# Performance work log

Hardware: AMD Instinct MI355X
Metric: run time of the kernel (lower is better)

## Reference

```python
import jax, jax.numpy as jnp
import numpy as np

C = 512
NUM_HEADS = 8
GROUPS = 32
EPS_GN = 1e-5
EPS_ATTN = 1e-6


def setup_inputs() -> dict:
    key = jax.random.key(0)
    ks = jax.random.split(key, 7)
    B, H, W = 8, 64, 64
    x = jax.random.normal(ks[0], (B, C, H, W), dtype=jnp.float32)
    # GroupNorm affine (torch default: weight=1, bias=0)
    norm_gamma = jnp.ones((C,), dtype=jnp.float32)
    norm_beta = jnp.zeros((C,), dtype=jnp.float32)
    # 1x1 conv weights stored as (out, in); torch Conv2d kaiming-ish scale
    qkv_w = jax.random.normal(ks[1], (3 * C, C), dtype=jnp.float32) * (1.0 / np.sqrt(C))
    qkv_b = jax.random.normal(ks[2], (3 * C,), dtype=jnp.float32) * 0.01
    proj_w = jax.random.normal(ks[3], (C, C), dtype=jnp.float32) * (1.0 / np.sqrt(C))
    proj_b = jax.random.normal(ks[4], (C,), dtype=jnp.float32) * 0.01
    return {"x": x, "norm_gamma": norm_gamma, "norm_beta": norm_beta,
            "qkv_w": qkv_w, "qkv_b": qkv_b, "proj_w": proj_w, "proj_b": proj_b}


def _group_norm(x, gamma, beta):
    B, Cc, H, W = x.shape
    xg = x.reshape(B, GROUPS, Cc // GROUPS, H, W)
    mean = xg.mean(axis=(2, 3, 4), keepdims=True)
    var = xg.var(axis=(2, 3, 4), keepdims=True)
    xn = (xg - mean) * jax.lax.rsqrt(var + EPS_GN)
    xn = xn.reshape(B, Cc, H, W)
    return xn * gamma[None, :, None, None] + beta[None, :, None, None]


def reference(x, norm_gamma, norm_beta, qkv_w, qkv_b, proj_w, proj_b):
    B, Cc, H, W = x.shape
    h, d = NUM_HEADS, Cc // NUM_HEADS
    N = H * W
    x_norm = _group_norm(x, norm_gamma, norm_beta)
    # 1x1 conv == channel GEMM
    qkv = jnp.einsum('bchw,oc->bohw', x_norm, qkv_w) + qkv_b[None, :, None, None]
    q, k, v = jnp.split(qkv, 3, axis=1)
    # (B, C, H, W) -> (B, h, N, d)
    def to_heads(t):
        return t.reshape(B, h, d, N).transpose(0, 1, 3, 2)
    q, k, v = to_heads(q), to_heads(k), to_heads(v)
    # phi(x) = elu(x) + 1
    q = jax.nn.elu(q) + 1.0
    k = jax.nn.elu(k) + 1.0
    kv = jnp.einsum('bhnd,bhne->bhde', k, v)          # (B,h,d,d)
    out = jnp.einsum('bhnd,bhde->bhne', q, kv)        # (B,h,N,d)
    denom = jnp.einsum('bhnd,bhd->bhn', q, k.sum(axis=2))
    out = out / (denom[..., None] + EPS_ATTN)
    # (B,h,N,d) -> (B,C,H,W)
    attn = out.transpose(0, 1, 3, 2).reshape(B, Cc, H, W)
    proj = jnp.einsum('bchw,oc->bohw', attn, proj_w) + proj_b[None, :, None, None]
    # dropout is identity at inference
    return x + proj
```

## Files before the change

kernel.cpp:

```cpp
#include <hip/hip_runtime.h>
#include <math.h>

#define BATCH   8
#define CCH     512
#define NHEADS  8
#define HD      64
#define NGROUPS 32
#define CPG     16
#define NSP     4096
#define O1      1536

typedef __attribute__((ext_vector_type(8))) short          short8;
typedef __attribute__((ext_vector_type(8))) unsigned short ushort8;
typedef __attribute__((ext_vector_type(4))) unsigned short ushort4v;
typedef __attribute__((ext_vector_type(4))) float          float4v;

#define GLOAD_LDS16(g, s) __builtin_amdgcn_global_load_lds(                   \
    (const __attribute__((address_space(1))) void*)(g),                       \
    (__attribute__((address_space(3))) void*)(s), 16, 0, 0)

__device__ __forceinline__ float phi_act(float v) {
    return v > 0.f ? v + 1.f : __expf(v);
}
__device__ __forceinline__ unsigned short f2bf(float f) {
    union { float f; unsigned int u; } c; c.f = f;
    unsigned int u = c.u;
    u += 0x7fffu + ((u >> 16) & 1u);
    return (unsigned short)(u >> 16);
}
__device__ __forceinline__ float bf2f(unsigned short s) {
    union { unsigned int u; float f; } c; c.u = ((unsigned int)s) << 16;
    return c.f;
}


__global__ __launch_bounds__(256) void gn_stats(const float* __restrict__ x,
                                                const float* __restrict__ gamma,
                                                const float* __restrict__ beta,
                                                float* __restrict__ ss) {
    const int bg = blockIdx.x;
    const int t  = threadIdx.x;
    const float* base = x + (size_t)bg * (CPG * NSP);
    float s = 0.f, s2 = 0.f;
    #pragma unroll 4
    for (int i = 0; i < 64; ++i) {
        float4 v = *(const float4*)(base + (i * 256 + t) * 4);
        s  += v.x + v.y + v.z + v.w;
        s2 += v.x * v.x + v.y * v.y + v.z * v.z + v.w * v.w;
    }
    __shared__ float r1[256], r2[256];
    r1[t] = s; r2[t] = s2;
    __syncthreads();
    for (int off = 128; off > 0; off >>= 1) {
        if (t < off) { r1[t] += r1[t + off]; r2[t] += r2[t + off]; }
        __syncthreads();
    }
    if (t < CPG) {
        const float inv = 1.f / 65536.f;
        float mean = r1[0] * inv;
        float var  = r2[0] * inv - mean * mean;
        float rstd = rsqrtf(var + 1e-5f);
        int b = bg / NGROUPS, g = bg % NGROUPS;
        int c = g * CPG + t;
        float sc = gamma[c] * rstd;
        float sh = beta[c] - mean * sc;
        ss[(b * CCH + c) * 2]     = sc;
        ss[(b * CCH + c) * 2 + 1] = sh;
    }
}

__global__ __launch_bounds__(256) void conv_w(const float* __restrict__ qw,
                                              const float* __restrict__ pw,
                                              unsigned short* __restrict__ qwb,
                                              unsigned short* __restrict__ pwb,
                                              float* __restrict__ ksum,
                                              float* __restrict__ den) {
    int i = (blockIdx.x * 256 + threadIdx.x) * 4;
    if (i < O1 * CCH) {
        float4 v = *(const float4*)(qw + i);
        unsigned short o[4] = {f2bf(v.x), f2bf(v.y), f2bf(v.z), f2bf(v.w)};
        *(uint2*)(qwb + i) = *(uint2*)o;
    } else {
        int j = i - O1 * CCH;
        float4 v = *(const float4*)(pw + j);
        unsigned short o[4] = {f2bf(v.x), f2bf(v.y), f2bf(v.z), f2bf(v.w)};
        *(uint2*)(pwb + j) = *(uint2*)o;
    }
    float4 z = {0.f, 0.f, 0.f, 0.f};
    if (blockIdx.x == 0) {
        #pragma unroll
        for (int l = 0; l < 4; ++l)
            *(float4*)(ksum + (l * 256 + threadIdx.x) * 4) = z;
    }
    if (blockIdx.x < 32)
        *(float4*)(den + (blockIdx.x * 256 + threadIdx.x) * 4) = z;
}

__global__ __launch_bounds__(256) void xnT_kernel(const float* __restrict__ x,
                                                  const float* __restrict__ ss,
                                                  unsigned short* __restrict__ xnT) {
    const int n0 = blockIdx.x * 64, c0 = blockIdx.y * 64, b = blockIdx.z;
    const int t = threadIdx.x;
    __shared__ float tile[64][65];
    const float* xb  = x + ((size_t)b * CCH + c0) * NSP + n0;
    const float* ssb = ss + b * CCH * 2;

    const int lr = t / 16, lc = (t % 16) * 4;
    #pragma unroll
    for (int j = 0; j < 4; ++j) {
        int cr = j * 16 + lr;
        float4 v = *(const float4*)(xb + (size_t)cr * NSP + lc);
        float sc = ssb[(c0 + cr) * 2], sh = ssb[(c0 + cr) * 2 + 1];
        tile[cr][lc + 0] = v.x * sc + sh;
        tile[cr][lc + 1] = v.y * sc + sh;
        tile[cr][lc + 2] = v.z * sc + sh;
        tile[cr][lc + 3] = v.w * sc + sh;
    }
    __syncthreads();
    #pragma unroll
    for (int j = 0; j < 2; ++j) {
        int wd = j * 256 + t;
        int n  = wd >> 3;
        int cb = (wd & 7) * 8;
        ushort8 o;
        #pragma unroll
        for (int i = 0; i < 8; ++i) o[i] = f2bf(tile[cb + i][n]);
        *(ushort8*)(xnT + ((size_t)b * NSP + n0 + n) * CCH + c0 + cb) = o;
    }
}

__global__ __launch_bounds__(256) void gemm_q(const unsigned short* __restrict__ A,
                                              const unsigned short* __restrict__ Bt,
                                              const float* __restrict__ bias,
                                              const float* __restrict__ ksum,
                                              unsigned short* __restrict__ qT,
                                              float* __restrict__ den) {
    const int n0 = blockIdx.x * 128;
    const int o0 = blockIdx.y * 128;
    const int b  = blockIdx.z;
    const int t  = threadIdx.x;
    const int wv = t >> 6, ln = t & 63;
    const int quad = ln >> 4, lm = ln & 15;
    const int wo = (wv >> 1) * 64, wn = (wv & 1) * 64;

    __shared__ __align__(16) unsigned short As[128 * 64];
    __shared__ __align__(16) unsigned short Bs[128 * 64];
    __shared__ float kss[128];

    if (t < 32)
        *(float4*)(kss + t * 4) = *(const float4*)(ksum + b * CCH + o0 + t * 4);

    float4v acc[4][4];
    #pragma unroll
    for (int i = 0; i < 4; ++i)
        #pragma unroll
        for (int j = 0; j < 4; ++j) acc[i][j] = {0.f, 0.f, 0.f, 0.f};

    const unsigned short* aBase = A + (size_t)o0 * CCH;
    const unsigned short* bBase = Bt + ((size_t)b * NSP + n0) * CCH;

    const int srow8 = ln >> 3;
    const int scs   = ((ln & 7) ^ srow8) * 8;
    const int lmp   = (lm & 7);

    for (int k0 = 0; k0 < CCH; k0 += 64) {
        __syncthreads();
        #pragma unroll
        for (int i = 0; i < 4; ++i) {
            int slab = wv + i * 4;
            GLOAD_LDS16(aBase + (size_t)(slab * 8 + srow8) * CCH + k0 + scs,
                        As + slab * 512);
            GLOAD_LDS16(bBase + (size_t)(slab * 8 + srow8) * CCH + k0 + scs,
                        Bs + slab * 512);
        }
        __syncthreads();
        #pragma unroll
        for (int kk = 0; kk < 2; ++kk) {
            const int sc8 = ((kk * 4 + quad) ^ lmp) * 8;
            short8 fw[4], fx[4];
            #pragma unroll
            for (int i = 0; i < 4; ++i)
                fw[i] = *(const short8*)(As + (wo + i * 16 + lm) * 64 + sc8);
            #pragma unroll
            for (int j = 0; j < 4; ++j)
                fx[j] = *(const short8*)(Bs + (wn + j * 16 + lm) * 64 + sc8);
            #pragma unroll
            for (int i = 0; i < 4; ++i)
                #pragma unroll
                for (int j = 0; j < 4; ++j)
                    acc[i][j] = __builtin_amdgcn_mfma_f32_16x16x32_bf16(
                        fw[i], fx[j], acc[i][j], 0, 0, 0);
        }
    }

    float denp[4] = {0.f, 0.f, 0.f, 0.f};
    #pragma unroll
    for (int i = 0; i < 4; ++i) {
        int ob = o0 + wo + i * 16 + quad * 4;
        float4 b4 = *(const float4*)(bias + ob);
        float bs[4] = {b4.x, b4.y, b4.z, b4.w};
        float4 k4 = *(const float4*)(kss + wo + i * 16 + quad * 4);
        float kf[4] = {k4.x, k4.y, k4.z, k4.w};
        #pragma unroll
        for (int j = 0; j < 4; ++j) {
            int n = n0 + wn + j * 16 + lm;
            ushort4v pk;
            #pragma unroll
            for (int r = 0; r < 4; ++r) {
                float qv = phi_act(acc[i][j][r] + bs[r]);
                pk[r] = f2bf(qv);
                denp[j] += qv * kf[r];
            }
            *(ushort4v*)(qT + ((size_t)b * NSP + n) * CCH + ob) = pk;
        }
    }
    #pragma unroll
    for (int j = 0; j < 4; ++j) {
        float s = denp[j];
        s += __shfl_xor(s, 16);
        s += __shfl_xor(s, 32);
        if (quad == 0)
            atomicAdd(den + (size_t)b * NSP + n0 + wn + j * 16 + lm, s);
    }
}

__global__ __launch_bounds__(256) void gemm_kv(const unsigned short* __restrict__ A,
                                               const unsigned short* __restrict__ Bt,
                                               const float* __restrict__ bias,
                                               float* __restrict__ ksum,
                                               float* __restrict__ kvp) {
    const int n0 = blockIdx.x * 128;
    const int h  = blockIdx.y;
    const int b  = blockIdx.z;
    const int t  = threadIdx.x;
    const int wv = t >> 6, ln = t & 63;
    const int quad = ln >> 4, lm = ln & 15;
    const int wo = (wv >> 1) * 64, wn = (wv & 1) * 64;

    __shared__ __align__(16) unsigned short sh[2 * 128 * 64];

    float4v acc[4][4];
    #pragma unroll
    for (int i = 0; i < 4; ++i)
        #pragma unroll
        for (int j = 0; j < 4; ++j) acc[i][j] = {0.f, 0.f, 0.f, 0.f};

    const unsigned short* aK = A + (size_t)(512 + h * 64) * CCH;
    const unsigned short* aV = A + (size_t)(1024 + h * 64) * CCH;
    const unsigned short* bBase = Bt + ((size_t)b * NSP + n0) * CCH;

    const int srow8 = ln >> 3;
    const int scs   = ((ln & 7) ^ srow8) * 8;
    const int lmp   = (lm & 7);

    for (int k0 = 0; k0 < CCH; k0 += 64) {
        __syncthreads();
        #pragma unroll
        for (int i = 0; i < 4; ++i) {
            int slab = wv + i * 4;
            const unsigned short* ab = (slab < 8)
                ? aK + (size_t)(slab * 8 + srow8) * CCH
                : aV + (size_t)((slab - 8) * 8 + srow8) * CCH;
            GLOAD_LDS16(ab + k0 + scs, sh + slab * 512);
            GLOAD_LDS16(bBase + (size_t)(slab * 8 + srow8) * CCH + k0 + scs,
                        sh + 8192 + slab * 512);
        }
        __syncthreads();
        #pragma unroll
        for (int kk = 0; kk < 2; ++kk) {
            const int sc8 = ((kk * 4 + quad) ^ lmp) * 8;
            short8 fw[4], fx[4];
            #pragma unroll
            for (int i = 0; i < 4; ++i)
                fw[i] = *(const short8*)(sh + (wo + i * 16 + lm) * 64 + sc8);
            #pragma unroll
            for (int j = 0; j < 4; ++j)
                fx[j] = *(const short8*)(sh + 8192 + (wn + j * 16 + lm) * 64 + sc8);
            #pragma unroll
            for (int i = 0; i < 4; ++i)
                #pragma unroll
                for (int j = 0; j < 4; ++j)
                    acc[i][j] = __builtin_amdgcn_mfma_f32_16x16x32_bf16(
                        fx[j], fw[i], acc[i][j], 0, 0, 0);
        }
    }

    __syncthreads();
    const bool isk = (wv < 2);
    const float* bptr = bias + (isk ? 512 : 1024) + h * 64;
    float ksp[4] = {0.f, 0.f, 0.f, 0.f};
    #pragma unroll
    for (int i = 0; i < 4; ++i) {
        float bs = bptr[i * 16 + lm];
        int row = wo + i * 16 + lm;
        #pragma unroll
        for (int j = 0; j < 4; ++j) {
            int n = wn + j * 16 + quad * 4;
            ushort4v pk;
            #pragma unroll
            for (int r = 0; r < 4; ++r) {
                float v = acc[i][j][r] + bs;
                if (isk) { v = phi_act(v); ksp[i] += v; }
                pk[r] = f2bf(v);
            }
            int idx = row * 128 + ((((n >> 3) ^ (row & 15)) << 3) | (n & 7));
            *(ushort4v*)(sh + idx) = pk;
        }
    }
    if (isk) {
        #pragma unroll
        for (int i = 0; i < 4; ++i) {
            float s = ksp[i];
            s += __shfl_xor(s, 16);
            s += __shfl_xor(s, 32);
            if (quad == 0)
                atomicAdd(ksum + b * CCH + h * 64 + i * 16 + lm, s);
        }
    }
    __syncthreads();

    const int wd = (wv >> 1) * 32, we = (wv & 1) * 32;
    float4v acc2[2][2];
    #pragma unroll
    for (int i = 0; i < 2; ++i)
        #pragma unroll
        for (int j = 0; j < 2; ++j) acc2[i][j] = {0.f, 0.f, 0.f, 0.f};

    #pragma unroll
    for (int ks = 0; ks < 4; ++ks) {
        short8 ka[2], vbf[2];
        #pragma unroll
        for (int i2 = 0; i2 < 2; ++i2) {
            int row = wd + i2 * 16 + lm;
            ka[i2] = *(const short8*)(sh + row * 128 +
                                      (((ks * 4 + quad) ^ (row & 15)) << 3));
        }
        #pragma unroll
        for (int j2 = 0; j2 < 2; ++j2) {
            int row = 64 + we + j2 * 16 + lm;
            vbf[j2] = *(const short8*)(sh + row * 128 +
                                       (((ks * 4 + quad) ^ (row & 15)) << 3));
        }
        #pragma unroll
        for (int i2 = 0; i2 < 2; ++i2)
            #pragma unroll
            for (int j2 = 0; j2 < 2; ++j2)
                acc2[i2][j2] = __builtin_amdgcn_mfma_f32_16x16x32_bf16(
                    vbf[j2], ka[i2], acc2[i2][j2], 0, 0, 0);
    }

    const int chunk = blockIdx.x;
    const int bh = b * 8 + h;
    #pragma unroll
    for (int i2 = 0; i2 < 2; ++i2)
        #pragma unroll
        for (int j2 = 0; j2 < 2; ++j2) {
            int d = wd + i2 * 16 + lm;
            int e = we + j2 * 16 + quad * 4;
            float4 r = {acc2[i2][j2][0], acc2[i2][j2][1],
                        acc2[i2][j2][2], acc2[i2][j2][3]};
            *(float4*)(kvp + ((size_t)(chunk * 64 + bh) * 64 + d) * 64 + e) = r;
        }
}

__global__ __launch_bounds__(256) void kv_reduce(const float* __restrict__ kvp,
                                                 unsigned short* __restrict__ kvTb) {
    int idx4 = (blockIdx.x * 256 + threadIdx.x) * 4;
    float4 s = {0.f, 0.f, 0.f, 0.f};
    #pragma unroll
    for (int p = 0; p < 32; ++p) {
        float4 v = *(const float4*)(kvp + (size_t)p * (64 * 64 * 64) + idx4);
        s.x += v.x; s.y += v.y; s.z += v.z; s.w += v.w;
    }
    ushort4v o = {f2bf(s.x), f2bf(s.y), f2bf(s.z), f2bf(s.w)};
    *(ushort4v*)(kvTb + idx4) = o;
}

__global__ __launch_bounds__(256) void kv_w(const unsigned short* __restrict__ kvTb,
                                            const unsigned short* __restrict__ pwb,
                                            unsigned short* __restrict__ Mw) {
    const int os = blockIdx.x * 128;
    const int bh = blockIdx.y;
    const int b = bh >> 3, h = bh & 7;
    const int t = threadIdx.x;
    const int wv = t >> 6, ln = t & 63;
    const int quad = ln >> 4, lm = ln & 15;

    __shared__ __align__(16) unsigned short kvs[64 * 64];

    {
        int d = t >> 2, e0 = (t & 3) * 16;
        const unsigned short* src = kvTb + (size_t)bh * 4096 + d * 64 + e0;
        int c0 = e0 >> 3;
        ushort8 v0 = *(const ushort8*)(src);
        ushort8 v1 = *(const ushort8*)(src + 8);
        *(ushort8*)(kvs + d * 64 + ((c0 ^ (d & 7)) << 3))       = v0;
        *(ushort8*)(kvs + d * 64 + (((c0 + 1) ^ (d & 7)) << 3)) = v1;
    }
    __syncthreads();

    short8 ka[4][2];
    #pragma unroll
    for (int i = 0; i < 4; ++i)
        #pragma unroll
        for (int kk = 0; kk < 2; ++kk) {
            int d = i * 16 + lm;
            ka[i][kk] = *(const short8*)(kvs + d * 64 +
                        (((kk * 4 + quad) ^ (lm & 7)) << 3));
        }
    short8 fw[2][2];
    #pragma unroll
    for (int j = 0; j < 2; ++j)
        #pragma unroll
        for (int kk = 0; kk < 2; ++kk) {
            int o = os + wv * 32 + j * 16 + lm;
            fw[j][kk] = *(const short8*)(pwb + (size_t)o * CCH + h * 64 +
                                         kk * 32 + quad * 8);
        }

    float4v acc[4][2];
    #pragma unroll
    for (int i = 0; i < 4; ++i)
        #pragma unroll
        for (int j = 0; j < 2; ++j) acc[i][j] = {0.f, 0.f, 0.f, 0.f};
    #pragma unroll
    for (int kk = 0; kk < 2; ++kk)
        #pragma unroll
        for (int i = 0; i < 4; ++i)
            #pragma unroll
            for (int j = 0; j < 2; ++j)
                acc[i][j] = __builtin_amdgcn_mfma_f32_16x16x32_bf16(
                    ka[i][kk], fw[j][kk], acc[i][j], 0, 0, 0);

    #pragma unroll
    for (int i = 0; i < 4; ++i)
        #pragma unroll
        for (int j = 0; j < 2; ++j) {
            int o = os + wv * 32 + j * 16 + lm;
            int c = h * 64 + i * 16 + quad * 4;
            ushort4v pk;
            #pragma unroll
            for (int r = 0; r < 4; ++r) pk[r] = f2bf(acc[i][j][r]);
            *(ushort4v*)(Mw + ((size_t)b * CCH + o) * CCH + c) = pk;
        }
}

__global__ __launch_bounds__(256) void gemm_proj(const unsigned short* __restrict__ Mw,
                                                 const unsigned short* __restrict__ Bt,
                                                 const float* __restrict__ bias,
                                                 const float* __restrict__ den,
                                                 const float* __restrict__ resid,
                                                 float* __restrict__ outF) {
    const int n0 = blockIdx.x * 128;
    const int o0 = blockIdx.y * 128;
    const int b  = blockIdx.z;
    const int t  = threadIdx.x;
    const int wv = t >> 6, ln = t & 63;
    const int quad = ln >> 4, lm = ln & 15;
    const int wo = (wv >> 1) * 64, wn = (wv & 1) * 64;

    __shared__ __align__(16) unsigned short As[128 * 64];
    __shared__ __align__(16) unsigned short Bs[128 * 64];

    float4v acc[4][4];
    #pragma unroll
    for (int i = 0; i < 4; ++i)
        #pragma unroll
        for (int j = 0; j < 4; ++j) acc[i][j] = {0.f, 0.f, 0.f, 0.f};

    const unsigned short* aBase = Mw + ((size_t)b * CCH + o0) * CCH;
    const unsigned short* bBase = Bt + ((size_t)b * NSP + n0) * CCH;

    const int srow8 = ln >> 3;
    const int scs   = ((ln & 7) ^ srow8) * 8;
    const int lmp   = (lm & 7);

    for (int k0 = 0; k0 < CCH; k0 += 64) {
        __syncthreads();
        #pragma unroll
        for (int i = 0; i < 4; ++i) {
            int slab = wv + i * 4;
            GLOAD_LDS16(aBase + (size_t)(slab * 8 + srow8) * CCH + k0 + scs,
                        As + slab * 512);
            GLOAD_LDS16(bBase + (size_t)(slab * 8 + srow8) * CCH + k0 + scs,
                        Bs + slab * 512);
        }
        __syncthreads();
        #pragma unroll
        for (int kk = 0; kk < 2; ++kk) {
            const int sc8 = ((kk * 4 + quad) ^ lmp) * 8;
            short8 fw[4], fx[4];
            #pragma unroll
            for (int i = 0; i < 4; ++i)
                fw[i] = *(const short8*)(As + (wo + i * 16 + lm) * 64 + sc8);
            #pragma unroll
            for (int j = 0; j < 4; ++j)
                fx[j] = *(const short8*)(Bs + (wn + j * 16 + lm) * 64 + sc8);
            #pragma unroll
            for (int i = 0; i < 4; ++i)
                #pragma unroll
                for (int j = 0; j < 4; ++j)
                    acc[i][j] = __builtin_amdgcn_mfma_f32_16x16x32_bf16(
                        fx[j], fw[i], acc[i][j], 0, 0, 0);
        }
    }

    float4v rden[4];
    #pragma unroll
    for (int j = 0; j < 4; ++j) {
        float4 dn = *(const float4*)(den + (size_t)b * NSP + n0 + wn +
                                     j * 16 + quad * 4);
        rden[j][0] = 1.f / (dn.x + 1e-6f);
        rden[j][1] = 1.f / (dn.y + 1e-6f);
        rden[j][2] = 1.f / (dn.z + 1e-6f);
        rden[j][3] = 1.f / (dn.w + 1e-6f);
    }
    #pragma unroll
    for (int i = 0; i < 4; ++i) {
        int o = o0 + wo + i * 16 + lm;
        float bs = bias[o];
        #pragma unroll
        for (int j = 0; j < 4; ++j) {
            int n = n0 + wn + j * 16 + quad * 4;
            size_t off = ((size_t)b * CCH + o) * NSP + n;
            float4 rv = *(const float4*)(resid + off);
            float4 w = {acc[i][j][0] * rden[j][0] + bs + rv.x,
                        acc[i][j][1] * rden[j][1] + bs + rv.y,
                        acc[i][j][2] * rden[j][2] + bs + rv.z,
                        acc[i][j][3] * rden[j][3] + bs + rv.w};
            *(float4*)(outF + off) = w;
        }
    }
}

extern "C" void kernel_launch(void* const* d_in, const int* in_sizes, int n_in,
                              void* d_out, int out_size, void* d_ws, size_t ws_size,
                              hipStream_t stream) {
    const float* x      = (const float*)d_in[0];
    const float* gamma  = (const float*)d_in[1];
    const float* beta   = (const float*)d_in[2];
    const float* qkv_w  = (const float*)d_in[3];
    const float* qkv_b  = (const float*)d_in[4];
    const float* proj_w = (const float*)d_in[5];
    const float* proj_b = (const float*)d_in[6];
    float* out = (float*)d_out;

    float* ws   = (float*)d_ws;
    float* ss   = ws;
    float* ksum = ss + 8192;
    float* den  = ksum + 4096;
    float* kvp  = den + 32768;
    unsigned short* xnT  = (unsigned short*)(kvp + (size_t)32 * 64 * 64 * 64);
    unsigned short* qT   = xnT + (size_t)BATCH * NSP * CCH;
    unsigned short* kvTb = qT  + (size_t)BATCH * NSP * CCH;
    unsigned short* Mw   = kvTb + (size_t)64 * 64 * 64;
    unsigned short* wqb  = Mw + (size_t)BATCH * CCH * CCH;
    unsigned short* wpb  = wqb + (size_t)O1 * CCH;

    gn_stats<<<BATCH * NGROUPS, 256, 0, stream>>>(x, gamma, beta, ss);
    conv_w<<<(O1 * CCH + CCH * CCH) / 4 / 256, 256, 0, stream>>>(qkv_w, proj_w, wqb, wpb, ksum, den);
    xnT_kernel<<<dim3(NSP / 64, CCH / 64, BATCH), 256, 0, stream>>>(x, ss, xnT);

    gemm_kv<<<dim3(NSP / 128, NHEADS, BATCH), 256, 0, stream>>>(wqb, xnT, qkv_b, ksum, kvp);
    gemm_q <<<dim3(NSP / 128, 4, BATCH), 256, 0, stream>>>(wqb, xnT, qkv_b, ksum, qT, den);

    kv_reduce<<<256, 256, 0, stream>>>(kvp, kvTb);
    kv_w<<<dim3(4, 64), 256, 0, stream>>>(kvTb, wpb, Mw);

    gemm_proj<<<dim3(NSP / 128, CCH / 128, BATCH), 256, 0, stream>>>(
        Mw, qT, proj_b, den, x, out);
}
```

Measured before the change: 283.3 us.

## Double-buffer GEMM K-loops, merge small kernels, move denominator out of gemm_q

The three bf16 GEMM kernels now use a double-buffered LDS pipeline with 32-wide K steps, so the global-to-LDS load of the next slice overlaps the MFMAs on the current one and each step needs one barrier instead of two. GroupNorm stats and weight conversion are merged into one launch, as are the kv reduction and a new per-row denominator pass. That pass recomputes q·ksum from the bf16 qT rather than using atomics in the gemm_q epilogue, which also removes the need to zero den. The trade-offs are more loop iterations with half the MFMA work per barrier, and the denominator now uses bf16-rounded q values.

```diff
diff --git a/kernel.cpp b/kernel.cpp
--- a/kernel.cpp
+++ b/kernel.cpp
@@ -34,12 +34,39 @@
 }
 
 
-__global__ __launch_bounds__(256) void gn_stats(const float* __restrict__ x,
-                                                const float* __restrict__ gamma,
-                                                const float* __restrict__ beta,
-                                                float* __restrict__ ss) {
-    const int bg = blockIdx.x;
-    const int t  = threadIdx.x;
+__global__ __launch_bounds__(256) void pre_kernel(const float* __restrict__ x,
+                                                  const float* __restrict__ gamma,
+                                                  const float* __restrict__ beta,
+                                                  const float* __restrict__ qw,
+                                                  const float* __restrict__ pw,
+                                                  unsigned short* __restrict__ qwb,
+                                                  unsigned short* __restrict__ pwb,
+                                                  float* __restrict__ ksum,
+                                                  float* __restrict__ ss) {
+    __shared__ float r1[256], r2[256];
+    const int bid = blockIdx.x;
+    const int t   = threadIdx.x;
+    if (bid < 1024) {
+        int i = (bid * 256 + t) * 4;
+        if (i < O1 * CCH) {
+            float4 v = *(const float4*)(qw + i);
+            unsigned short o[4] = {f2bf(v.x), f2bf(v.y), f2bf(v.z), f2bf(v.w)};
+            *(uint2*)(qwb + i) = *(uint2*)o;
+        } else {
+            int j = i - O1 * CCH;
+            float4 v = *(const float4*)(pw + j);
+            unsigned short o[4] = {f2bf(v.x), f2bf(v.y), f2bf(v.z), f2bf(v.w)};
+            *(uint2*)(pwb + j) = *(uint2*)o;
+        }
+        if (bid == 0) {
+            float4 z = {0.f, 0.f, 0.f, 0.f};
+            #pragma unroll
+            for (int l = 0; l < 4; ++l)
+                *(float4*)(ksum + (l * 256 + t) * 4) = z;
+        }
+        return;
+    }
+    const int bg = bid - 1024;
     const float* base = x + (size_t)bg * (CPG * NSP);
     float s = 0.f, s2 = 0.f;
     #pragma unroll 4
@@ -48,7 +75,6 @@
         s  += v.x + v.y + v.z + v.w;
         s2 += v.x * v.x + v.y * v.y + v.z * v.z + v.w * v.w;
     }
-    __shared__ float r1[256], r2[256];
     r1[t] = s; r2[t] = s2;
     __syncthreads();
     for (int off = 128; off > 0; off >>= 1) {
@@ -69,33 +95,6 @@
     }
 }
 
-__global__ __launch_bounds__(256) void conv_w(const float* __restrict__ qw,
-                                              const float* __restrict__ pw,
-                                              unsigned short* __restrict__ qwb,
-                                              unsigned short* __restrict__ pwb,
-                                              float* __restrict__ ksum,
-                                              float* __restrict__ den) {
-    int i = (blockIdx.x * 256 + threadIdx.x) * 4;
-    if (i < O1 * CCH) {
-        float4 v = *(const float4*)(qw + i);
-        unsigned short o[4] = {f2bf(v.x), f2bf(v.y), f2bf(v.z), f2bf(v.w)};
-        *(uint2*)(qwb + i) = *(uint2*)o;
-    } else {
-        int j = i - O1 * CCH;
-        float4 v = *(const float4*)(pw + j);
-        unsigned short o[4] = {f2bf(v.x), f2bf(v.y), f2bf(v.z), f2bf(v.w)};
-        *(uint2*)(pwb + j) = *(uint2*)o;
-    }
-    float4 z = {0.f, 0.f, 0.f, 0.f};
-    if (blockIdx.x == 0) {
-        #pragma unroll
-        for (int l = 0; l < 4; ++l)
-            *(float4*)(ksum + (l * 256 + threadIdx.x) * 4) = z;
-    }
-    if (blockIdx.x < 32)
-        *(float4*)(den + (blockIdx.x * 256 + threadIdx.x) * 4) = z;
-}
-
 __global__ __launch_bounds__(256) void xnT_kernel(const float* __restrict__ x,
                                                   const float* __restrict__ ss,
                                                   unsigned short* __restrict__ xnT) {
@@ -126,101 +125,6 @@
         #pragma unroll
         for (int i = 0; i < 8; ++i) o[i] = f2bf(tile[cb + i][n]);
         *(ushort8*)(xnT + ((size_t)b * NSP + n0 + n) * CCH + c0 + cb) = o;
-    }
-}
-
-__global__ __launch_bounds__(256) void gemm_q(const unsigned short* __restrict__ A,
-                                              const unsigned short* __restrict__ Bt,
-                                              const float* __restrict__ bias,
-                                              const float* __restrict__ ksum,
-                                              unsigned short* __restrict__ qT,
-                                              float* __restrict__ den) {
-    const int n0 = blockIdx.x * 128;
-    const int o0 = blockIdx.y * 128;
-    const int b  = blockIdx.z;
-    const int t  = threadIdx.x;
-    const int wv = t >> 6, ln = t & 63;
-    const int quad = ln >> 4, lm = ln & 15;
-    const int wo = (wv >> 1) * 64, wn = (wv & 1) * 64;
-
-    __shared__ __align__(16) unsigned short As[128 * 64];
-    __shared__ __align__(16) unsigned short Bs[128 * 64];
-    __shared__ float kss[128];
-
-    if (t < 32)
-        *(float4*)(kss + t * 4) = *(const float4*)(ksum + b * CCH + o0 + t * 4);
-
-    float4v acc[4][4];
-    #pragma unroll
-    for (int i = 0; i < 4; ++i)
-        #pragma unroll
-        for (int j = 0; j < 4; ++j) acc[i][j] = {0.f, 0.f, 0.f, 0.f};
-
-    const unsigned short* aBase = A + (size_t)o0 * CCH;
-    const unsigned short* bBase = Bt + ((size_t)b * NSP + n0) * CCH;
-
-    const int srow8 = ln >> 3;
-    const int scs   = ((ln & 7) ^ srow8) * 8;
-    const int lmp   = (lm & 7);
-
-    for (int k0 = 0; k0 < CCH; k0 += 64) {
-        __syncthreads();
-        #pragma unroll
-        for (int i = 0; i < 4; ++i) {
-            int slab = wv + i * 4;
-            GLOAD_LDS16(aBase + (size_t)(slab * 8 + srow8) * CCH + k0 + scs,
-                        As + slab * 512);
-            GLOAD_LDS16(bBase + (size_t)(slab * 8 + srow8) * CCH + k0 + scs,
-                        Bs + slab * 512);
-        }
-        __syncthreads();
-        #pragma unroll
-        for (int kk = 0; kk < 2; ++kk) {
-            const int sc8 = ((kk * 4 + quad) ^ lmp) * 8;
-            short8 fw[4], fx[4];
-            #pragma unroll
-            for (int i = 0; i < 4; ++i)
-                fw[i] = *(const short8*)(As + (wo + i * 16 + lm) * 64 + sc8);
-            #pragma unroll
-            for (int j = 0; j < 4; ++j)
-                fx[j] = *(const short8*)(Bs + (wn + j * 16 + lm) * 64 + sc8);
-            #pragma unroll
-            for (int i = 0; i < 4; ++i)
-                #pragma unroll
-                for (int j = 0; j < 4; ++j)
-                    acc[i][j] = __builtin_amdgcn_mfma_f32_16x16x32_bf16(
-                        fw[i], fx[j], acc[i][j], 0, 0, 0);
-        }
-    }
-
-    float denp[4] = {0.f, 0.f, 0.f, 0.f};
-    #pragma unroll
-    for (int i = 0; i < 4; ++i) {
-        int ob = o0 + wo + i * 16 + quad * 4;
-        float4 b4 = *(const float4*)(bias + ob);
-        float bs[4] = {b4.x, b4.y, b4.z, b4.w};
-        float4 k4 = *(const float4*)(kss + wo + i * 16 + quad * 4);
-        float kf[4] = {k4.x, k4.y, k4.z, k4.w};
-        #pragma unroll
-        for (int j = 0; j < 4; ++j) {
-            int n = n0 + wn + j * 16 + lm;
-            ushort4v pk;
-            #pragma unroll
-            for (int r = 0; r < 4; ++r) {
-                float qv = phi_act(acc[i][j][r] + bs[r]);
-                pk[r] = f2bf(qv);
-                denp[j] += qv * kf[r];
-            }
-            *(ushort4v*)(qT + ((size_t)b * NSP + n) * CCH + ob) = pk;
-        }
-    }
-    #pragma unroll
-    for (int j = 0; j < 4; ++j) {
-        float s = denp[j];
-        s += __shfl_xor(s, 16);
-        s += __shfl_xor(s, 32);
-        if (quad == 0)
-            atomicAdd(den + (size_t)b * NSP + n0 + wn + j * 16 + lm, s);
     }
 }
 
@@ -237,7 +141,7 @@
     const int quad = ln >> 4, lm = ln & 15;
     const int wo = (wv >> 1) * 64, wn = (wv & 1) * 64;
 
-    __shared__ __align__(16) unsigned short sh[2 * 128 * 64];
+    __shared__ __align__(16) unsigned short sh[16384];
 
     float4v acc[4][4];
     #pragma unroll
@@ -249,40 +153,68 @@
     const unsigned short* aV = A + (size_t)(1024 + h * 64) * CCH;
     const unsigned short* bBase = Bt + ((size_t)b * NSP + n0) * CCH;
 
-    const int srow8 = ln >> 3;
-    const int scs   = ((ln & 7) ^ srow8) * 8;
-    const int lmp   = (lm & 7);
-
-    for (int k0 = 0; k0 < CCH; k0 += 64) {
+    const int srow = ln >> 2;
+    const int gcs  = (((ln & 3) ^ (srow & 3))) * 8;
+    const int slab0 = wv * 2, slab1 = slab0 + 1;
+    const unsigned short* aR0 = ((slab0 < 4)
+        ? aK + (size_t)(slab0 * 16 + srow) * CCH
+        : aV + (size_t)((slab0 - 4) * 16 + srow) * CCH) + gcs;
+    const unsigned short* aR1 = ((slab1 < 4)
+        ? aK + (size_t)(slab1 * 16 + srow) * CCH
+        : aV + (size_t)((slab1 - 4) * 16 + srow) * CCH) + gcs;
+    const unsigned short* bR0 = bBase + (size_t)(slab0 * 16 + srow) * CCH + gcs;
+    const unsigned short* bR1 = bBase + (size_t)(slab1 * 16 + srow) * CCH + gcs;
+    const int dA0 = slab0 * 512, dA1 = slab1 * 512;
+    const int sc  = (quad ^ (lm & 3)) * 8;
+
+    GLOAD_LDS16(aR0, sh + dA0);
+    GLOAD_LDS16(aR1, sh + dA1);
+    GLOAD_LDS16(bR0, sh + 4096 + dA0);
+    GLOAD_LDS16(bR1, sh + 4096 + dA1);
+    __syncthreads();
+
+    int cur = 0;
+    for (int step = 0; step < 15; ++step) {
+        const int nb = (cur ^ 1) * 8192;
+        const int k1 = (step + 1) * 32;
+        GLOAD_LDS16(aR0 + k1, sh + nb + dA0);
+        GLOAD_LDS16(aR1 + k1, sh + nb + dA1);
+        GLOAD_LDS16(bR0 + k1, sh + nb + 4096 + dA0);
+        GLOAD_LDS16(bR1 + k1, sh + nb + 4096 + dA1);
+        const unsigned short* Ab = sh + cur * 8192;
+        const unsigned short* Bb = Ab + 4096;
+        short8 fw[4], fx[4];
+        #pragma unroll
+        for (int i = 0; i < 4; ++i)
+            fw[i] = *(const short8*)(Ab + (wo + i * 16 + lm) * 32 + sc);
+        #pragma unroll
+        for (int j = 0; j < 4; ++j)
+            fx[j] = *(const short8*)(Bb + (wn + j * 16 + lm) * 32 + sc);
+        #pragma unroll
+        for (int i = 0; i < 4; ++i)
+            #pragma unroll
+            for (int j = 0; j < 4; ++j)
+                acc[i][j] = __builtin_amdgcn_mfma_f32_16x16x32_bf16(
+                    fx[j], fw[i], acc[i][j], 0, 0, 0);
         __syncthreads();
-        #pragma unroll
-        for (int i = 0; i < 4; ++i) {
-            int slab = wv + i * 4;
-            const unsigned short* ab = (slab < 8)
-                ? aK + (size_t)(slab * 8 + srow8) * CCH
-                : aV + (size_t)((slab - 8) * 8 + srow8) * CCH;
-            GLOAD_LDS16(ab + k0 + scs, sh + slab * 512);
-            GLOAD_LDS16(bBase + (size_t)(slab * 8 + srow8) * CCH + k0 + scs,
-                        sh + 8192 + slab * 512);
-        }
-        __syncthreads();
-        #pragma unroll
-        for (int kk = 0; kk < 2; ++kk) {
-            const int sc8 = ((kk * 4 + quad) ^ lmp) * 8;
-            short8 fw[4], fx[4];
-            #pragma unroll
-            for (int i = 0; i < 4; ++i)
-                fw[i] = *(const short8*)(sh + (wo + i * 16 + lm) * 64 + sc8);
+        cur ^= 1;
+    }
+    {
+        const unsigned short* Ab = sh + cur * 8192;
+        const unsigned short* Bb = Ab + 4096;
+        short8 fw[4], fx[4];
+        #pragma unroll
+        for (int i = 0; i < 4; ++i)
+            fw[i] = *(const short8*)(Ab + (wo + i * 16 + lm) * 32 + sc);
+        #pragma unroll
+        for (int j = 0; j < 4; ++j)
+            fx[j] = *(const short8*)(Bb + (wn + j * 16 + lm) * 32 + sc);
+        #pragma unroll
+        for (int i = 0; i < 4; ++i)
             #pragma unroll
             for (int j = 0; j < 4; ++j)
-                fx[j] = *(const short8*)(sh + 8192 + (wn + j * 16 + lm) * 64 + sc8);
-            #pragma unroll
-            for (int i = 0; i < 4; ++i)
-                #pragma unroll
-                for (int j = 0; j < 4; ++j)
-                    acc[i][j] = __builtin_amdgcn_mfma_f32_16x16x32_bf16(
-                        fx[j], fw[i], acc[i][j], 0, 0, 0);
-        }
+                acc[i][j] = __builtin_amdgcn_mfma_f32_16x16x32_bf16(
+                    fx[j], fw[i], acc[i][j], 0, 0, 0);
     }
 
     __syncthreads();
@@ -363,17 +295,143 @@
         }
 }
 
-__global__ __launch_bounds__(256) void kv_reduce(const float* __restrict__ kvp,
-                                                 unsigned short* __restrict__ kvTb) {
-    int idx4 = (blockIdx.x * 256 + threadIdx.x) * 4;
-    float4 s = {0.f, 0.f, 0.f, 0.f};
-    #pragma unroll
-    for (int p = 0; p < 32; ++p) {
-        float4 v = *(const float4*)(kvp + (size_t)p * (64 * 64 * 64) + idx4);
-        s.x += v.x; s.y += v.y; s.z += v.z; s.w += v.w;
-    }
-    ushort4v o = {f2bf(s.x), f2bf(s.y), f2bf(s.z), f2bf(s.w)};
-    *(ushort4v*)(kvTb + idx4) = o;
+__global__ __launch_bounds__(256) void gemm_q(const unsigned short* __restrict__ A,
+                                              const unsigned short* __restrict__ Bt,
+                                              const float* __restrict__ bias,
+                                              unsigned short* __restrict__ qT) {
+    const int n0 = blockIdx.x * 128;
+    const int o0 = blockIdx.y * 128;
+    const int b  = blockIdx.z;
+    const int t  = threadIdx.x;
+    const int wv = t >> 6, ln = t & 63;
+    const int quad = ln >> 4, lm = ln & 15;
+    const int wo = (wv >> 1) * 64, wn = (wv & 1) * 64;
+
+    __shared__ __align__(16) unsigned short sh[16384];
+
+    float4v acc[4][4];
+    #pragma unroll
+    for (int i = 0; i < 4; ++i)
+        #pragma unroll
+        for (int j = 0; j < 4; ++j) acc[i][j] = {0.f, 0.f, 0.f, 0.f};
+
+    const unsigned short* aBase = A + (size_t)o0 * CCH;
+    const unsigned short* bBase = Bt + ((size_t)b * NSP + n0) * CCH;
+
+    const int srow = ln >> 2;
+    const int gcs  = (((ln & 3) ^ (srow & 3))) * 8;
+    const int slab0 = wv * 2, slab1 = slab0 + 1;
+    const unsigned short* aR0 = aBase + (size_t)(slab0 * 16 + srow) * CCH + gcs;
+    const unsigned short* aR1 = aBase + (size_t)(slab1 * 16 + srow) * CCH + gcs;
+    const unsigned short* bR0 = bBase + (size_t)(slab0 * 16 + srow) * CCH + gcs;
+    const unsigned short* bR1 = bBase + (size_t)(slab1 * 16 + srow) * CCH + gcs;
+    const int dA0 = slab0 * 512, dA1 = slab1 * 512;
+    const int sc  = (quad ^ (lm & 3)) * 8;
+
+    GLOAD_LDS16(aR0, sh + dA0);
+    GLOAD_LDS16(aR1, sh + dA1);
+    GLOAD_LDS16(bR0, sh + 4096 + dA0);
+    GLOAD_LDS16(bR1, sh + 4096 + dA1);
+    __syncthreads();
+
+    int cur = 0;
+    for (int step = 0; step < 15; ++step) {
+        const int nb = (cur ^ 1) * 8192;
+        const int k1 = (step + 1) * 32;
+        GLOAD_LDS16(aR0 + k1, sh + nb + dA0);
+        GLOAD_LDS16(aR1 + k1, sh + nb + dA1);
+        GLOAD_LDS16(bR0 + k1, sh + nb + 4096 + dA0);
+        GLOAD_LDS16(bR1 + k1, sh + nb + 4096 + dA1);
+        const unsigned short* Ab = sh + cur * 8192;
+        const unsigned short* Bb = Ab + 4096;
+        short8 fw[4], fx[4];
+        #pragma unroll
+        for (int i = 0; i < 4; ++i)
+            fw[i] = *(const short8*)(Ab + (wo + i * 16 + lm) * 32 + sc);
+        #pragma unroll
+        for (int j = 0; j < 4; ++j)
+            fx[j] = *(const short8*)(Bb + (wn + j * 16 + lm) * 32 + sc);
+        #pragma unroll
+        for (int i = 0; i < 4; ++i)
+            #pragma unroll
+            for (int j = 0; j < 4; ++j)
+                acc[i][j] = __builtin_amdgcn_mfma_f32_16x16x32_bf16(
+                    fw[i], fx[j], acc[i][j], 0, 0, 0);
+        __syncthreads();
+        cur ^= 1;
+    }
+    {
+        const unsigned short* Ab = sh + cur * 8192;
+        const unsigned short* Bb = Ab + 4096;
+        short8 fw[4], fx[4];
+        #pragma unroll
+        for (int i = 0; i < 4; ++i)
+            fw[i] = *(const short8*)(Ab + (wo + i * 16 + lm) * 32 + sc);
+        #pragma unroll
+        for (int j = 0; j < 4; ++j)
+            fx[j] = *(const short8*)(Bb + (wn + j * 16 + lm) * 32 + sc);
+        #pragma unroll
+        for (int i = 0; i < 4; ++i)
+            #pragma unroll
+            for (int j = 0; j < 4; ++j)
+                acc[i][j] = __builtin_amdgcn_mfma_f32_16x16x32_bf16(
+                    fw[i], fx[j], acc[i][j], 0, 0, 0);
+    }
+
+    #pragma unroll
+    for (int i = 0; i < 4; ++i) {
+        int ob = o0 + wo + i * 16 + quad * 4;
+        float4 b4 = *(const float4*)(bias + ob);
+        float bs[4] = {b4.x, b4.y, b4.z, b4.w};
+        #pragma unroll
+        for (int j = 0; j < 4; ++j) {
+            int n = n0 + wn + j * 16 + lm;
+            ushort4v pk;
+            #pragma unroll
+            for (int r = 0; r < 4; ++r)
+                pk[r] = f2bf(phi_act(acc[i][j][r] + bs[r]));
+            *(ushort4v*)(qT + ((size_t)b * NSP + n) * CCH + ob) = pk;
+        }
+    }
+}
+
+__global__ __launch_bounds__(256) void mid_kernel(const float* __restrict__ kvp,
+                                                  unsigned short* __restrict__ kvTb,
+                                                  const unsigned short* __restrict__ qT,
+                                                  const float* __restrict__ ksum,
+                                                  float* __restrict__ den) {
+    const int t = threadIdx.x;
+    if (blockIdx.x < 256) {
+        int idx4 = (blockIdx.x * 256 + t) * 4;
+        float4 s = {0.f, 0.f, 0.f, 0.f};
+        #pragma unroll
+        for (int p = 0; p < 32; ++p) {
+            float4 v = *(const float4*)(kvp + (size_t)p * (64 * 64 * 64) + idx4);
+            s.x += v.x; s.y += v.y; s.z += v.z; s.w += v.w;
+        }
+        ushort4v o = {f2bf(s.x), f2bf(s.y), f2bf(s.z), f2bf(s.w)};
+        *(ushort4v*)(kvTb + idx4) = o;
+        return;
+    }
+    const int bid = blockIdx.x - 256;
+    const int b  = bid >> 5;
+    const int n0 = (bid & 31) * 128;
+    const int wv = t >> 6, ln = t & 63;
+    float kf[8];
+    #pragma unroll
+    for (int l = 0; l < 8; ++l) kf[l] = ksum[b * CCH + ln * 8 + l];
+    #pragma unroll 4
+    for (int it = 0; it < 32; ++it) {
+        int n = n0 + wv * 32 + it;
+        short8 qv = *(const short8*)(qT + ((size_t)b * NSP + n) * CCH + ln * 8);
+        float s = 0.f;
+        #pragma unroll
+        for (int l = 0; l < 8; ++l)
+            s += bf2f((unsigned short)qv[l]) * kf[l];
+        #pragma unroll
+        for (int off = 1; off < 64; off <<= 1) s += __shfl_xor(s, off);
+        if (ln == 0) den[(size_t)b * NSP + n] = s;
+    }
 }
 
 __global__ __launch_bounds__(256) void kv_w(const unsigned short* __restrict__ kvTb,
@@ -459,8 +517,7 @@
     const int quad = ln >> 4, lm = ln & 15;
     const int wo = (wv >> 1) * 64, wn = (wv & 1) * 64;
 
-    __shared__ __align__(16) unsigned short As[128 * 64];
-    __shared__ __align__(16) unsigned short Bs[128 * 64];
+    __shared__ __align__(16) unsigned short sh[16384];
 
     float4v acc[4][4];
     #pragma unroll
@@ -471,38 +528,64 @@
     const unsigned short* aBase = Mw + ((size_t)b * CCH + o0) * CCH;
     const unsigned short* bBase = Bt + ((size_t)b * NSP + n0) * CCH;
 
-    const int srow8 = ln >> 3;
-    const int scs   = ((ln & 7) ^ srow8) * 8;
-    const int lmp   = (lm & 7);
-
-    for (int k0 = 0; k0 < CCH; k0 += 64) {
+    const int srow = ln >> 2;
+    const int gcs  = (((ln & 3) ^ (srow & 3))) * 8;
+    const int slab0 = wv * 2, slab1 = slab0 + 1;
+    const unsigned short* aR0 = aBase + (size_t)(slab0 * 16 + srow) * CCH + gcs;
+    const unsigned short* aR1 = aBase + (size_t)(slab1 * 16 + srow) * CCH + gcs;
+    const unsigned short* bR0 = bBase + (size_t)(slab0 * 16 + srow) * CCH + gcs;
+    const unsigned short* bR1 = bBase + (size_t)(slab1 * 16 + srow) * CCH + gcs;
+    const int dA0 = slab0 * 512, dA1 = slab1 * 512;
+    const int sc  = (quad ^ (lm & 3)) * 8;
+
+    GLOAD_LDS16(aR0, sh + dA0);
+    GLOAD_LDS16(aR1, sh + dA1);
+    GLOAD_LDS16(bR0, sh + 4096 + dA0);
+    GLOAD_LDS16(bR1, sh + 4096 + dA1);
+    __syncthreads();
+
+    int cur = 0;
+    for (int step = 0; step < 15; ++step) {
+        const int nb = (cur ^ 1) * 8192;
+        const int k1 = (step + 1) * 32;
+        GLOAD_LDS16(aR0 + k1, sh + nb + dA0);
+        GLOAD_LDS16(aR1 + k1, sh + nb + dA1);
+        GLOAD_LDS16(bR0 + k1, sh + nb + 4096 + dA0);
+        GLOAD_LDS16(bR1 + k1, sh + nb + 4096 + dA1);
+        const unsigned short* Ab = sh + cur * 8192;
+        const unsigned short* Bb = Ab + 4096;
+        short8 fw[4], fx[4];
+        #pragma unroll
+        for (int i = 0; i < 4; ++i)
+            fw[i] = *(const short8*)(Ab + (wo + i * 16 + lm) * 32 + sc);
+        #pragma unroll
+        for (int j = 0; j < 4; ++j)
+            fx[j] = *(const short8*)(Bb + (wn + j * 16 + lm) * 32 + sc);
+        #pragma unroll
+        for (int i = 0; i < 4; ++i)
+            #pragma unroll
+            for (int j = 0; j < 4; ++j)
+                acc[i][j] = __builtin_amdgcn_mfma_f32_16x16x32_bf16(
+                    fx[j], fw[i], acc[i][j], 0, 0, 0);
         __syncthreads();
-        #pragma unroll
-        for (int i = 0; i < 4; ++i) {
-            int slab = wv + i * 4;
-            GLOAD_LDS16(aBase + (size_t)(slab * 8 + srow8) * CCH + k0 + scs,
-                        As + slab * 512);
-            GLOAD_LDS16(bBase + (size_t)(slab * 8 + srow8) * CCH + k0 + scs,
-                        Bs + slab * 512);
-        }
-        __syncthreads();
-        #pragma unroll
-        for (int kk = 0; kk < 2; ++kk) {
-            const int sc8 = ((kk * 4 + quad) ^ lmp) * 8;
-            short8 fw[4], fx[4];
-            #pragma unroll
-            for (int i = 0; i < 4; ++i)
-                fw[i] = *(const short8*)(As + (wo + i * 16 + lm) * 64 + sc8);
+        cur ^= 1;
+    }
+    {
+        const unsigned short* Ab = sh + cur * 8192;
+        const unsigned short* Bb = Ab + 4096;
+        short8 fw[4], fx[4];
+        #pragma unroll
+        for (int i = 0; i < 4; ++i)
+            fw[i] = *(const short8*)(Ab + (wo + i * 16 + lm) * 32 + sc);
+        #pragma unroll
+        for (int j = 0; j < 4; ++j)
+            fx[j] = *(const short8*)(Bb + (wn + j * 16 + lm) * 32 + sc);
+        #pragma unroll
+        for (int i = 0; i < 4; ++i)
             #pragma unroll
             for (int j = 0; j < 4; ++j)
-                fx[j] = *(const short8*)(Bs + (wn + j * 16 + lm) * 64 + sc8);
-            #pragma unroll
-            for (int i = 0; i < 4; ++i)
-                #pragma unroll
-                for (int j = 0; j < 4; ++j)
-                    acc[i][j] = __builtin_amdgcn_mfma_f32_16x16x32_bf16(
-                        fx[j], fw[i], acc[i][j], 0, 0, 0);
-        }
+                acc[i][j] = __builtin_amdgcn_mfma_f32_16x16x32_bf16(
+                    fx[j], fw[i], acc[i][j], 0, 0, 0);
     }
 
     float4v rden[4];
@@ -557,14 +640,15 @@
     unsigned short* wqb  = Mw + (size_t)BATCH * CCH * CCH;
     unsigned short* wpb  = wqb + (size_t)O1 * CCH;
 
-    gn_stats<<<BATCH * NGROUPS, 256, 0, stream>>>(x, gamma, beta, ss);
-    conv_w<<<(O1 * CCH + CCH * CCH) / 4 / 256, 256, 0, stream>>>(qkv_w, proj_w, wqb, wpb, ksum, den);
+    pre_kernel<<<1280, 256, 0, stream>>>(x, gamma, beta, qkv_w, proj_w,
+                                         wqb, wpb, ksum, ss);
     xnT_kernel<<<dim3(NSP / 64, CCH / 64, BATCH), 256, 0, stream>>>(x, ss, xnT);
 
-    gemm_kv<<<dim3(NSP / 128, NHEADS, BATCH), 256, 0, stream>>>(wqb, xnT, qkv_b, ksum, kvp);
-    gemm_q <<<dim3(NSP / 128, 4, BATCH), 256, 0, stream>>>(wqb, xnT, qkv_b, ksum, qT, den);
-
-    kv_reduce<<<256, 256, 0, stream>>>(kvp, kvTb);
+    gemm_kv<<<dim3(NSP / 128, NHEADS, BATCH), 256, 0, stream>>>(
+        wqb, xnT, qkv_b, ksum, kvp);
+    gemm_q <<<dim3(NSP / 128, 4, BATCH), 256, 0, stream>>>(wqb, xnT, qkv_b, qT);
+
+    mid_kernel<<<512, 256, 0, stream>>>(kvp, kvTb, qT, ksum, den);
     kv_w<<<dim3(4, 64), 256, 0, stream>>>(kvTb, wpb, Mw);
 
     gemm_proj<<<dim3(NSP / 128, CCH / 128, BATCH), 256, 0, stream>>>(
```

After: 285.8 us. Within noise of the previous version (+0.9%).
